# Kernel optimization log

Hardware: AMD Instinct MI355X
Metric: run time of the kernel (lower is better)

## Reference

```python
import jax, jax.numpy as jnp
import numpy as np

T, B, C = 512, 64, 512
ALPHA = 0.6        # blend coefficient from __init__
TAU = 10.0         # LIF tau
VTH = 1.0          # LIF v_threshold (v_reset = 0, hard reset)
BN_EPS = 1e-5


def spike_fn(x):
    # forward heaviside: spike = (v - v_th >= 0)
    return (x >= 0.0).astype(x.dtype)


def setup_inputs() -> dict:
    key = jax.random.key(0)
    ks = jax.random.split(key, 7)
    x = jax.random.normal(ks[0], (T, B, C), dtype=jnp.float32)
    conv_w = jax.random.normal(ks[1], (C, C, 3), dtype=jnp.float32) / np.sqrt(3.0 * C)
    conv_b = jax.random.normal(ks[2], (C,), dtype=jnp.float32) * 0.01
    bn_gamma = 0.5 + jax.random.uniform(ks[3], (C,), dtype=jnp.float32)
    bn_beta = jax.random.normal(ks[4], (C,), dtype=jnp.float32) * 0.1
    bn_mean = jax.random.normal(ks[5], (C,), dtype=jnp.float32) * 0.1
    bn_var = 0.5 + jax.random.uniform(ks[6], (C,), dtype=jnp.float32)
    return {"x": x, "conv_w": conv_w, "conv_b": conv_b,
            "bn_gamma": bn_gamma, "bn_beta": bn_beta,
            "bn_mean": bn_mean, "bn_var": bn_var}


def reference(x, conv_w, conv_b, bn_gamma, bn_beta, bn_mean, bn_var):
    # x: (T, B, C). Conv1d(k=3, pad=1) on a length-1 sequence reduces to a
    # dense matmul with the middle kernel tap: out = prev @ w[:,:,1].T + b.
    w1 = conv_w[:, :, 1]                      # (C_out, C_in)
    inv_std = bn_gamma * jax.lax.rsqrt(bn_var + BN_EPS)   # fused BN scale
    Bsz, Csz = x.shape[1], x.shape[2]

    def step(carry, x_t):
        prev, v = carry                        # prev: (B, C), v: (B, C) membrane
        conv = jnp.einsum('bc,dc->bd', prev, w1) + conv_b
        bn = (conv - bn_mean) * inv_std + bn_beta
        # LIF (decay_input=True, v_reset=0): v += (x - v) / tau
        v = v + (bn - v) / TAU
        s = spike_fn(v - VTH)
        v = v * (1.0 - s)                      # hard reset to 0
        new = (1.0 - ALPHA) * x_t + ALPHA * s  # alpha blend
        return (new, v), new                   # prev_state detached in torch; no-op for fwd

    init = (jnp.zeros((Bsz, Csz), x.dtype), jnp.zeros((Bsz, Csz), x.dtype))
    _, out = jax.lax.scan(step, init, x)       # out: (T, B, C)
    return out
```

## Files before the change

### kernel.cpp

```cpp
#include <hip/hip_runtime.h>
#include <stdint.h>

#define T_STEPS 512
#define BATCH 64
#define CH 512

using short8 = __attribute__((ext_vector_type(8))) short;
using f32x4  = __attribute__((ext_vector_type(4))) float;

__device__ __forceinline__ unsigned short f2b(float f) {
    union { float f; unsigned u; } c; c.f = f;
    unsigned r = (c.u + 0x7FFFu + ((c.u >> 16) & 1u)) >> 16;
    return (unsigned short)r;
}
__device__ __forceinline__ float b2f(unsigned short h) {
    union { unsigned u; float f; } c; c.u = ((unsigned)h) << 16;
    return c.f;
}

__global__ void prep(const float* __restrict__ cw, const float* __restrict__ cb,
                     const float* __restrict__ gamma, const float* __restrict__ beta,
                     const float* __restrict__ mean, const float* __restrict__ var,
                     unsigned short* __restrict__ wb,
                     float* __restrict__ wt,
                     float* __restrict__ isb,
                     float* __restrict__ k0p,
                     int* __restrict__ flag) {
    int idx = blockIdx.x * 256 + threadIdx.x;
    if (idx == 0) *flag = 0x7fffffff;
    if (idx >= CH * CH) return;
    int d = idx >> 9, c = idx & 511;
    float is = gamma[d] * rsqrtf(var[d] + 1e-5f);
    float w = cw[((size_t)d * CH + c) * 3 + 1];
    wb[idx] = f2b(0.04f * is * w);
    wt[(size_t)c * CH + d] = w;
    if (c == 0) {
        isb[d] = is;
        k0p[d] = 0.1f * ((cb[d] - mean[d]) * is + beta[d]);
    }
}

#define GBM 128
#define GBN 256
#define PADK 40

__global__ __launch_bounds__(512, 4) void gemm_fused(
    const float* __restrict__ Xp,
    const unsigned short* __restrict__ wbp,
    const float* __restrict__ k0p,
    unsigned short* __restrict__ Wbuf,
    float* __restrict__ outp,
    int Mc)
{
    __shared__ __align__(16) unsigned short As[2][GBM][PADK];
    __shared__ __align__(16) unsigned short Bs[2][GBN][PADK];
    int tid = threadIdx.x;
    int lane = tid & 63, wid = tid >> 6;
    int wm = wid >> 2, wn = wid & 3;
    int i0 = blockIdx.x * GBM;
    int n0 = blockIdx.y * GBN;
    int fm = lane & 15, fq = lane >> 4;
    int kq = fq * 8;
    bool wout = (blockIdx.y == 0);

    int ar = tid >> 2;
    int ak = (tid & 3) * 8;
    int brr = tid >> 1;
    int bk = (tid & 1) * 16;

    int grow = i0 + ar;
    bool arv = grow < Mc;
    int growc = arv ? grow : (Mc - 1);
    const float* xrow = &Xp[(size_t)growc * CH + ak];
    float* orow = &outp[(size_t)grow * CH + ak];
    const unsigned short* brow = &wbp[(size_t)(n0 + brr) * CH + bk];

    f32x4 acc[4][4] = {};

    {
        float4 a0 = *(const float4*)&xrow[0];
        float4 a1 = *(const float4*)&xrow[4];
        short8 av;
        av[0]=f2b(a0.x); av[1]=f2b(a0.y); av[2]=f2b(a0.z); av[3]=f2b(a0.w);
        av[4]=f2b(a1.x); av[5]=f2b(a1.y); av[6]=f2b(a1.z); av[7]=f2b(a1.w);
        *(short8*)&As[0][ar][ak] = av;
        short8 b0 = *(const short8*)&brow[0];
        short8 b1 = *(const short8*)&brow[8];
        *(short8*)&Bs[0][brr][bk]     = b0;
        *(short8*)&Bs[0][brr][bk + 8] = b1;
        if (wout && arv) {
            *(float4*)&orow[0] = make_float4(0.4f*a0.x, 0.4f*a0.y, 0.4f*a0.z, 0.4f*a0.w);
            *(float4*)&orow[4] = make_float4(0.4f*a1.x, 0.4f*a1.y, 0.4f*a1.z, 0.4f*a1.w);
        }
    }
    __syncthreads();

    for (int ks = 0; ks < 16; ++ks) {
        int cur = ks & 1;
        int kn = (ks + 1) * 32;
        float4 na0, na1;
        short8 nb0, nb1;
        if (kn < 512) {
            na0 = *(const float4*)&xrow[kn];
            na1 = *(const float4*)&xrow[kn + 4];
            nb0 = *(const short8*)&brow[kn];
            nb1 = *(const short8*)&brow[kn + 8];
        }
        short8 af[4], bfr[4];
        #pragma unroll
        for (int i = 0; i < 4; ++i)
            af[i] = *(const short8*)&As[cur][wm * 64 + i * 16 + fm][kq];
        #pragma unroll
        for (int j = 0; j < 4; ++j)
            bfr[j] = *(const short8*)&Bs[cur][wn * 64 + j * 16 + fm][kq];
        #pragma unroll
        for (int i = 0; i < 4; ++i)
            #pragma unroll
            for (int j = 0; j < 4; ++j)
                acc[i][j] = __builtin_amdgcn_mfma_f32_16x16x32_bf16(af[i], bfr[j], acc[i][j], 0, 0, 0);
        if (kn < 512) {
            short8 av;
            av[0]=f2b(na0.x); av[1]=f2b(na0.y); av[2]=f2b(na0.z); av[3]=f2b(na0.w);
            av[4]=f2b(na1.x); av[5]=f2b(na1.y); av[6]=f2b(na1.z); av[7]=f2b(na1.w);
            *(short8*)&As[cur ^ 1][ar][ak] = av;
            *(short8*)&Bs[cur ^ 1][brr][bk]     = nb0;
            *(short8*)&Bs[cur ^ 1][brr][bk + 8] = nb1;
            if (wout && arv) {
                *(float4*)&orow[kn]     = make_float4(0.4f*na0.x, 0.4f*na0.y, 0.4f*na0.z, 0.4f*na0.w);
                *(float4*)&orow[kn + 4] = make_float4(0.4f*na1.x, 0.4f*na1.y, 0.4f*na1.z, 0.4f*na1.w);
            }
        }
        __syncthreads();
    }

    float b0e[4];
    #pragma unroll
    for (int j = 0; j < 4; ++j) b0e[j] = k0p[n0 + wn * 64 + j * 16 + fm];
    #pragma unroll
    for (int i = 0; i < 4; ++i)
        #pragma unroll
        for (int r = 0; r < 4; ++r) {
            int row = i0 + wm * 64 + i * 16 + fq * 4 + r;
            if (row < Mc) {
                #pragma unroll
                for (int j = 0; j < 4; ++j) {
                    int col = n0 + wn * 64 + j * 16 + fm;
                    Wbuf[(size_t)row * CH + col] = f2b(acc[i][j][r] + b0e[j]);
                }
            }
        }
}

__device__ __forceinline__ short8 wload(const unsigned short* Wbuf, int t, int a0, int b, int c0) {
    int r = t - 1 - a0; if (r < 0) r = 0;
    return *(const short8*)&Wbuf[((size_t)r * BATCH + b) * CH + c0];
}

__global__ __launch_bounds__(512) void scan_all(
    const unsigned short* __restrict__ Wbuf,
    const float* __restrict__ k0p,
    const float* __restrict__ vcin,
    float* __restrict__ vcout,
    int* __restrict__ flag,
    int t0, int a0, int segs, int chunk_idx)
{
    const float F = 1.1790184577738595e-3f;
    __shared__ float Ssh[8][CH];
    int b = blockIdx.x;
    int wid = threadIdx.x >> 6;
    int lane = threadIdx.x & 63;
    int c0 = lane * 8;
    int seg = wid;
    bool active = seg < segs;
    int tstart = t0 + seg * 64;

    float B0[8];
    #pragma unroll
    for (int k = 0; k < 8; ++k) B0[k] = k0p[c0 + k];

    if (active) {
        float S[8] = {};
        short8 pz[4];
        #pragma unroll
        for (int p = 0; p < 4; ++p) pz[p] = wload(Wbuf, tstart + p, a0, b, c0);
        for (int ii = 0; ii < 64; ii += 4) {
            #pragma unroll
            for (int p = 0; p < 4; ++p) {
                int t = tstart + ii + p;
                short8 zv = pz[p];
                int tn = ii + p + 4;
                if (tn < 64) pz[p] = wload(Wbuf, tstart + tn, a0, b, c0);
                #pragma unroll
                for (int k = 0; k < 8; ++k) {
                    float wv = (t == 0) ? B0[k] : b2f((unsigned short)zv[k]);
                    S[k] = fmaf(0.9f, S[k], wv);
                }
            }
        }
        #pragma unroll
        for (int k = 0; k < 8; ++k) Ssh[seg][c0 + k] = S[k];
    }
    __syncthreads();

    float v[8];
    if (t0 == 0) {
        #pragma unroll
        for (int k = 0; k < 8; ++k) v[k] = 0.0f;
    } else {
        const float* vp = &vcin[(size_t)b * CH + c0];
        float4 v0 = *(const float4*)&vp[0], v1 = *(const float4*)&vp[4];
        v[0]=v0.x; v[1]=v0.y; v[2]=v0.z; v[3]=v0.w; v[4]=v1.x; v[5]=v1.y; v[6]=v1.z; v[7]=v1.w;
    }
    for (int u = 0; u < seg; ++u) {
        #pragma unroll
        for (int k = 0; k < 8; ++k) v[k] = fmaf(v[k], F, Ssh[u][c0 + k]);
    }

    if (active) {
        bool anyhit = false;
        short8 pz[4];
        #pragma unroll
        for (int p = 0; p < 4; ++p) pz[p] = wload(Wbuf, tstart + p, a0, b, c0);
        for (int ii = 0; ii < 64; ii += 4) {
            #pragma unroll
            for (int p = 0; p < 4; ++p) {
                int t = tstart + ii + p;
                short8 zv = pz[p];
                int tn = ii + p + 4;
                if (tn < 64) pz[p] = wload(Wbuf, tstart + tn, a0, b, c0);
                float m = -1e30f;
                #pragma unroll
                for (int k = 0; k < 8; ++k) {
                    float wv = (t == 0) ? B0[k] : b2f((unsigned short)zv[k]);
                    v[k] = fmaf(0.9f, v[k], wv);
                    m = fmaxf(m, v[k]);
                }
                anyhit |= (m >= 0.995f);
            }
        }
        if (__ballot(anyhit) != 0ULL && lane == 0) atomicMin(flag, chunk_idx);
        if (seg == segs - 1) {
            float* vp = &vcout[(size_t)b * CH + c0];
            *(float4*)&vp[0] = make_float4(v[0], v[1], v[2], v[3]);
            *(float4*)&vp[4] = make_float4(v[4], v[5], v[6], v[7]);
        }
    }
}

__global__ __launch_bounds__(64) void seq_fix(
    const float* __restrict__ x,
    const float* __restrict__ wt,
    const unsigned short* __restrict__ Wbuf,
    const float* __restrict__ isb,
    const float* __restrict__ k0p,
    const int* __restrict__ flag,
    const float* __restrict__ vcin,
    float* __restrict__ out,
    float* __restrict__ v_state,
    unsigned long long* __restrict__ s_state,
    int t0, int t1, int a0, int chunk_idx, int save_state)
{
    int fl = *flag;
    if (fl > chunk_idx) return;
    int b = blockIdx.x;
    int lane = threadIdx.x;
    int c0 = lane * 8;

    float is6[8], B0[8];
    #pragma unroll
    for (int k = 0; k < 8; ++k) {
        is6[k] = 0.06f * isb[c0 + k];
        B0[k]  = k0p[c0 + k];
    }

    float v[8];
    unsigned long long mk[8];
    if (t0 == 0) {
        #pragma unroll
        for (int k = 0; k < 8; ++k) v[k] = 0.0f;
        #pragma unroll
        for (int j = 0; j < 8; ++j) mk[j] = 0ULL;
    } else if (fl == chunk_idx) {
        #pragma unroll
        for (int k = 0; k < 8; ++k) v[k] = vcin[(size_t)b * CH + c0 + k];
        #pragma unroll
        for (int j = 0; j < 8; ++j) mk[j] = 0ULL;
    } else {
        #pragma unroll
        for (int k = 0; k < 8; ++k) v[k] = v_state[(size_t)b * CH + c0 + k];
        #pragma unroll
        for (int j = 0; j < 8; ++j) mk[j] = s_state[b * 8 + j];
    }

    float xc[8]; short8 wc;
    {
        const float4* xp = (const float4*)&x[((size_t)t0 * BATCH + b) * CH + c0];
        float4 x0 = xp[0], x1 = xp[1];
        xc[0]=x0.x; xc[1]=x0.y; xc[2]=x0.z; xc[3]=x0.w; xc[4]=x1.x; xc[5]=x1.y; xc[6]=x1.z; xc[7]=x1.w;
        wc = wload(Wbuf, t0, a0, b, c0);
    }
    for (int t = t0; t < t1; ++t) {
        float xn[8]; short8 wn_;
        if (t + 1 < t1) {
            const float4* xp = (const float4*)&x[((size_t)(t + 1) * BATCH + b) * CH + c0];
            float4 x0 = xp[0], x1 = xp[1];
            xn[0]=x0.x; xn[1]=x0.y; xn[2]=x0.z; xn[3]=x0.w; xn[4]=x1.x; xn[5]=x1.y; xn[6]=x1.z; xn[7]=x1.w;
            wn_ = wload(Wbuf, t + 1, a0, b, c0);
        }
        float acc[8] = {};
        unsigned long long anym = mk[0]|mk[1]|mk[2]|mk[3]|mk[4]|mk[5]|mk[6]|mk[7];
        if (anym) {
            #pragma unroll
            for (int j = 0; j < 8; ++j) {
                unsigned long long m = mk[j];
                while (m) {
                    int l = __builtin_ctzll(m); m &= m - 1;
                    const float4* wr = (const float4*)&wt[(size_t)(l * 8 + j) * CH + c0];
                    float4 w0 = wr[0], w1 = wr[1];
                    acc[0]+=w0.x; acc[1]+=w0.y; acc[2]+=w0.z; acc[3]+=w0.w;
                    acc[4]+=w1.x; acc[5]+=w1.y; acc[6]+=w1.z; acc[7]+=w1.w;
                }
            }
        }
        bool s[8];
        #pragma unroll
        for (int k = 0; k < 8; ++k) {
            float wv = (t == 0) ? B0[k] : b2f((unsigned short)wc[k]);
            float vv = fmaf(0.9f, v[k], fmaf(is6[k], acc[k], wv));
            s[k] = (vv >= 1.0f);
            v[k] = s[k] ? 0.0f : vv;
        }
        float4* op = (float4*)&out[((size_t)t * BATCH + b) * CH + c0];
        op[0] = make_float4(fmaf(0.4f,xc[0],s[0]?0.6f:0.f), fmaf(0.4f,xc[1],s[1]?0.6f:0.f),
                            fmaf(0.4f,xc[2],s[2]?0.6f:0.f), fmaf(0.4f,xc[3],s[3]?0.6f:0.f));
        op[1] = make_float4(fmaf(0.4f,xc[4],s[4]?0.6f:0.f), fmaf(0.4f,xc[5],s[5]?0.6f:0.f),
                            fmaf(0.4f,xc[6],s[6]?0.6f:0.f), fmaf(0.4f,xc[7],s[7]?0.6f:0.f));
        #pragma unroll
        for (int j = 0; j < 8; ++j) mk[j] = __ballot(s[j]);
        #pragma unroll
        for (int k = 0; k < 8; ++k) xc[k] = xn[k];
        wc = wn_;
    }
    if (save_state) {
        #pragma unroll
        for (int k = 0; k < 8; ++k) v_state[(size_t)b * CH + c0 + k] = v[k];
        if (lane < 8) s_state[b * 8 + lane] = mk[lane];
    }
}

extern "C" void kernel_launch(void* const* d_in, const int* in_sizes, int n_in,
                              void* d_out, int out_size, void* d_ws, size_t ws_size,
                              hipStream_t stream) {
    const float* x     = (const float*)d_in[0];
    const float* cw    = (const float*)d_in[1];
    const float* cb    = (const float*)d_in[2];
    const float* gamma = (const float*)d_in[3];
    const float* beta  = (const float*)d_in[4];
    const float* mean  = (const float*)d_in[5];
    const float* var   = (const float*)d_in[6];
    float* out = (float*)d_out;

    char* ws = (char*)d_ws;
    size_t off = 0;
    auto alloc = [&](size_t bytes) -> char* {
        char* p = ws + off;
        off = (off + bytes + 255) & ~(size_t)255;
        return p;
    };
    unsigned short* wb = (unsigned short*)alloc((size_t)CH * CH * 2);
    float* wt  = (float*)alloc((size_t)CH * CH * 4);
    float* isb = (float*)alloc(CH * 4);
    float* k0p = (float*)alloc(CH * 4);
    int* flag  = (int*)alloc(256);
    float* vst = (float*)alloc((size_t)BATCH * CH * 4);
    unsigned long long* sst = (unsigned long long*)alloc(BATCH * 8 * 8);
    float* vca = (float*)alloc((size_t)BATCH * CH * 4);
    float* vcb = (float*)alloc((size_t)BATCH * CH * 4);
    unsigned short* Wbuf = (unsigned short*)(ws + off);

    size_t avail = (ws_size > off) ? ws_size - off : 0;
    long rows = (long)(avail / ((size_t)BATCH * CH * 2));
    long cs = ((rows - 1) / 64) * 64;
    if (cs > T_STEPS) cs = T_STEPS;
    if (cs < 64) cs = 64;
    int CS = (int)cs;

    hipLaunchKernelGGL(prep, dim3((CH * CH + 255) / 256), dim3(256), 0, stream,
                       cw, cb, gamma, beta, mean, var, wb, wt, isb, k0p, flag);

    float *vin = vca, *vout = vcb;
    int k = 0;
    for (int t0 = 0; t0 < T_STEPS; t0 += CS, ++k) {
        int t1 = t0 + CS; if (t1 > T_STEPS) t1 = T_STEPS;
        int a0 = (t0 == 0) ? 0 : t0 - 1;
        int gend = (t1 == T_STEPS) ? T_STEPS : t1 - 1;
        int Mc = (gend - a0) * BATCH;
        hipLaunchKernelGGL(gemm_fused, dim3((Mc + GBM - 1) / GBM, 2), dim3(512), 0, stream,
                           x + (size_t)a0 * BATCH * CH, wb, k0p, Wbuf,
                           out + (size_t)a0 * BATCH * CH, Mc);
        int segs = (t1 - t0) / 64;
        hipLaunchKernelGGL(scan_all, dim3(BATCH), dim3(512), 0, stream,
                           Wbuf, k0p, vin, vout, flag, t0, a0, segs, k);
        hipLaunchKernelGGL(seq_fix, dim3(BATCH), dim3(64), 0, stream,
                           x, wt, Wbuf, isb, k0p, flag, vin, out, vst, sst,
                           t0, t1, a0, k, (t1 < T_STEPS) ? 1 : 0);
        float* tmp = vin; vin = vout; vout = tmp;
    }
}
```

Measured before the change: 77.47 us.

## Widen GEMM tile to full N and replace scan second pass with prefix-max bound

The GEMM now covers all 512 output columns per block, so each X row is loaded and converted to bf16 once instead of twice, at the cost of a doubled accumulator set and larger LDS with lower occupancy. The scan kernel drops its second sequential pass over Wbuf. It tracks a running max of the zero-start partial sum, bounds the threshold check with 0.9*max(v,0)+P, and computes the end state as v*F+S. The bound is conservative and could flag extra chunks for the sequential fix path. The bf16 conversion also switches to the HIP intrinsic.

Result: slower. 276.7 us (+257.2%).

```diff
diff --git a/kernel.cpp b/kernel.cpp
--- a/kernel.cpp
+++ b/kernel.cpp
@@ -1,4 +1,5 @@
 #include <hip/hip_runtime.h>
+#include <hip/hip_bf16.h>
 #include <stdint.h>
 
 #define T_STEPS 512
@@ -9,9 +10,9 @@
 using f32x4  = __attribute__((ext_vector_type(4))) float;
 
 __device__ __forceinline__ unsigned short f2b(float f) {
-    union { float f; unsigned u; } c; c.f = f;
-    unsigned r = (c.u + 0x7FFFu + ((c.u >> 16) & 1u)) >> 16;
-    return (unsigned short)r;
+    union { __hip_bfloat16 h; unsigned short u; } c;
+    c.h = __float2bfloat16(f);
+    return c.u;
 }
 __device__ __forceinline__ float b2f(unsigned short h) {
     union { unsigned u; float f; } c; c.u = ((unsigned)h) << 16;
@@ -41,10 +42,9 @@
 }
 
 #define GBM 128
-#define GBN 256
 #define PADK 40
 
-__global__ __launch_bounds__(512, 4) void gemm_fused(
+__global__ __launch_bounds__(512, 2) void gemm_fused(
     const float* __restrict__ Xp,
     const unsigned short* __restrict__ wbp,
     const float* __restrict__ k0p,
@@ -53,44 +53,45 @@
     int Mc)
 {
     __shared__ __align__(16) unsigned short As[2][GBM][PADK];
-    __shared__ __align__(16) unsigned short Bs[2][GBN][PADK];
+    __shared__ __align__(16) unsigned short Bs[2][512][PADK];
     int tid = threadIdx.x;
     int lane = tid & 63, wid = tid >> 6;
     int wm = wid >> 2, wn = wid & 3;
     int i0 = blockIdx.x * GBM;
-    int n0 = blockIdx.y * GBN;
     int fm = lane & 15, fq = lane >> 4;
     int kq = fq * 8;
-    bool wout = (blockIdx.y == 0);
 
     int ar = tid >> 2;
     int ak = (tid & 3) * 8;
-    int brr = tid >> 1;
-    int bk = (tid & 1) * 16;
 
     int grow = i0 + ar;
     bool arv = grow < Mc;
     int growc = arv ? grow : (Mc - 1);
     const float* xrow = &Xp[(size_t)growc * CH + ak];
     float* orow = &outp[(size_t)grow * CH + ak];
-    const unsigned short* brow = &wbp[(size_t)(n0 + brr) * CH + bk];
-
-    f32x4 acc[4][4] = {};
+    const unsigned short* brow = &wbp[(size_t)ar * CH + ak];
+
+    f32x4 acc[4][8] = {};
+
+    float4 sa0, sa1;
+    short8 sb[4];
 
     {
-        float4 a0 = *(const float4*)&xrow[0];
-        float4 a1 = *(const float4*)&xrow[4];
+        sa0 = *(const float4*)&xrow[0];
+        sa1 = *(const float4*)&xrow[4];
+        #pragma unroll
+        for (int p = 0; p < 4; ++p)
+            sb[p] = *(const short8*)&brow[(size_t)p * 128 * CH];
         short8 av;
-        av[0]=f2b(a0.x); av[1]=f2b(a0.y); av[2]=f2b(a0.z); av[3]=f2b(a0.w);
-        av[4]=f2b(a1.x); av[5]=f2b(a1.y); av[6]=f2b(a1.z); av[7]=f2b(a1.w);
+        av[0]=f2b(sa0.x); av[1]=f2b(sa0.y); av[2]=f2b(sa0.z); av[3]=f2b(sa0.w);
+        av[4]=f2b(sa1.x); av[5]=f2b(sa1.y); av[6]=f2b(sa1.z); av[7]=f2b(sa1.w);
         *(short8*)&As[0][ar][ak] = av;
-        short8 b0 = *(const short8*)&brow[0];
-        short8 b1 = *(const short8*)&brow[8];
-        *(short8*)&Bs[0][brr][bk]     = b0;
-        *(short8*)&Bs[0][brr][bk + 8] = b1;
-        if (wout && arv) {
-            *(float4*)&orow[0] = make_float4(0.4f*a0.x, 0.4f*a0.y, 0.4f*a0.z, 0.4f*a0.w);
-            *(float4*)&orow[4] = make_float4(0.4f*a1.x, 0.4f*a1.y, 0.4f*a1.z, 0.4f*a1.w);
+        #pragma unroll
+        for (int p = 0; p < 4; ++p)
+            *(short8*)&Bs[0][ar + p * 128][ak] = sb[p];
+        if (arv) {
+            *(float4*)&orow[0] = make_float4(0.4f*sa0.x, 0.4f*sa0.y, 0.4f*sa0.z, 0.4f*sa0.w);
+            *(float4*)&orow[4] = make_float4(0.4f*sa1.x, 0.4f*sa1.y, 0.4f*sa1.z, 0.4f*sa1.w);
         }
     }
     __syncthreads();
@@ -98,44 +99,44 @@
     for (int ks = 0; ks < 16; ++ks) {
         int cur = ks & 1;
         int kn = (ks + 1) * 32;
-        float4 na0, na1;
-        short8 nb0, nb1;
         if (kn < 512) {
-            na0 = *(const float4*)&xrow[kn];
-            na1 = *(const float4*)&xrow[kn + 4];
-            nb0 = *(const short8*)&brow[kn];
-            nb1 = *(const short8*)&brow[kn + 8];
-        }
-        short8 af[4], bfr[4];
+            sa0 = *(const float4*)&xrow[kn];
+            sa1 = *(const float4*)&xrow[kn + 4];
+            #pragma unroll
+            for (int p = 0; p < 4; ++p)
+                sb[p] = *(const short8*)&brow[(size_t)p * 128 * CH + kn];
+        }
+        short8 af[4], bfr[8];
         #pragma unroll
         for (int i = 0; i < 4; ++i)
             af[i] = *(const short8*)&As[cur][wm * 64 + i * 16 + fm][kq];
         #pragma unroll
-        for (int j = 0; j < 4; ++j)
-            bfr[j] = *(const short8*)&Bs[cur][wn * 64 + j * 16 + fm][kq];
+        for (int j = 0; j < 8; ++j)
+            bfr[j] = *(const short8*)&Bs[cur][wn * 128 + j * 16 + fm][kq];
         #pragma unroll
         for (int i = 0; i < 4; ++i)
             #pragma unroll
-            for (int j = 0; j < 4; ++j)
+            for (int j = 0; j < 8; ++j)
                 acc[i][j] = __builtin_amdgcn_mfma_f32_16x16x32_bf16(af[i], bfr[j], acc[i][j], 0, 0, 0);
         if (kn < 512) {
             short8 av;
-            av[0]=f2b(na0.x); av[1]=f2b(na0.y); av[2]=f2b(na0.z); av[3]=f2b(na0.w);
-            av[4]=f2b(na1.x); av[5]=f2b(na1.y); av[6]=f2b(na1.z); av[7]=f2b(na1.w);
+            av[0]=f2b(sa0.x); av[1]=f2b(sa0.y); av[2]=f2b(sa0.z); av[3]=f2b(sa0.w);
+            av[4]=f2b(sa1.x); av[5]=f2b(sa1.y); av[6]=f2b(sa1.z); av[7]=f2b(sa1.w);
             *(short8*)&As[cur ^ 1][ar][ak] = av;
-            *(short8*)&Bs[cur ^ 1][brr][bk]     = nb0;
-            *(short8*)&Bs[cur ^ 1][brr][bk + 8] = nb1;
-            if (wout && arv) {
-                *(float4*)&orow[kn]     = make_float4(0.4f*na0.x, 0.4f*na0.y, 0.4f*na0.z, 0.4f*na0.w);
-                *(float4*)&orow[kn + 4] = make_float4(0.4f*na1.x, 0.4f*na1.y, 0.4f*na1.z, 0.4f*na1.w);
+            #pragma unroll
+            for (int p = 0; p < 4; ++p)
+                *(short8*)&Bs[cur ^ 1][ar + p * 128][ak] = sb[p];
+            if (arv) {
+                *(float4*)&orow[kn]     = make_float4(0.4f*sa0.x, 0.4f*sa0.y, 0.4f*sa0.z, 0.4f*sa0.w);
+                *(float4*)&orow[kn + 4] = make_float4(0.4f*sa1.x, 0.4f*sa1.y, 0.4f*sa1.z, 0.4f*sa1.w);
             }
         }
         __syncthreads();
     }
 
-    float b0e[4];
-    #pragma unroll
-    for (int j = 0; j < 4; ++j) b0e[j] = k0p[n0 + wn * 64 + j * 16 + fm];
+    float b0e[8];
+    #pragma unroll
+    for (int j = 0; j < 8; ++j) b0e[j] = k0p[wn * 128 + j * 16 + fm];
     #pragma unroll
     for (int i = 0; i < 4; ++i)
         #pragma unroll
@@ -143,8 +144,8 @@
             int row = i0 + wm * 64 + i * 16 + fq * 4 + r;
             if (row < Mc) {
                 #pragma unroll
-                for (int j = 0; j < 4; ++j) {
-                    int col = n0 + wn * 64 + j * 16 + fm;
+                for (int j = 0; j < 8; ++j) {
+                    int col = wn * 128 + j * 16 + fm;
                     Wbuf[(size_t)row * CH + col] = f2b(acc[i][j][r] + b0e[j]);
                 }
             }
@@ -167,10 +168,9 @@
     const float F = 1.1790184577738595e-3f;
     __shared__ float Ssh[8][CH];
     int b = blockIdx.x;
-    int wid = threadIdx.x >> 6;
+    int seg = threadIdx.x >> 6;
     int lane = threadIdx.x & 63;
     int c0 = lane * 8;
-    int seg = wid;
     bool active = seg < segs;
     int tstart = t0 + seg * 64;
 
@@ -178,8 +178,11 @@
     #pragma unroll
     for (int k = 0; k < 8; ++k) B0[k] = k0p[c0 + k];
 
+    float S[8] = {};
+    float P[8];
+    #pragma unroll
+    for (int k = 0; k < 8; ++k) P[k] = -1e30f;
     if (active) {
-        float S[8] = {};
         short8 pz[4];
         #pragma unroll
         for (int p = 0; p < 4; ++p) pz[p] = wload(Wbuf, tstart + p, a0, b, c0);
@@ -194,6 +197,7 @@
                 for (int k = 0; k < 8; ++k) {
                     float wv = (t == 0) ? B0[k] : b2f((unsigned short)zv[k]);
                     S[k] = fmaf(0.9f, S[k], wv);
+                    P[k] = fmaxf(P[k], S[k]);
                 }
             }
         }
@@ -217,32 +221,18 @@
     }
 
     if (active) {
-        bool anyhit = false;
-        short8 pz[4];
-        #pragma unroll
-        for (int p = 0; p < 4; ++p) pz[p] = wload(Wbuf, tstart + p, a0, b, c0);
-        for (int ii = 0; ii < 64; ii += 4) {
-            #pragma unroll
-            for (int p = 0; p < 4; ++p) {
-                int t = tstart + ii + p;
-                short8 zv = pz[p];
-                int tn = ii + p + 4;
-                if (tn < 64) pz[p] = wload(Wbuf, tstart + tn, a0, b, c0);
-                float m = -1e30f;
-                #pragma unroll
-                for (int k = 0; k < 8; ++k) {
-                    float wv = (t == 0) ? B0[k] : b2f((unsigned short)zv[k]);
-                    v[k] = fmaf(0.9f, v[k], wv);
-                    m = fmaxf(m, v[k]);
-                }
-                anyhit |= (m >= 0.995f);
-            }
-        }
-        if (__ballot(anyhit) != 0ULL && lane == 0) atomicMin(flag, chunk_idx);
+        bool hit = false;
+        #pragma unroll
+        for (int k = 0; k < 8; ++k)
+            hit |= (fmaf(0.9f, fmaxf(v[k], 0.0f), P[k]) >= 0.995f);
+        if (__ballot(hit) != 0ULL && lane == 0) atomicMin(flag, chunk_idx);
         if (seg == segs - 1) {
             float* vp = &vcout[(size_t)b * CH + c0];
-            *(float4*)&vp[0] = make_float4(v[0], v[1], v[2], v[3]);
-            *(float4*)&vp[4] = make_float4(v[4], v[5], v[6], v[7]);
+            float ve[8];
+            #pragma unroll
+            for (int k = 0; k < 8; ++k) ve[k] = fmaf(v[k], F, S[k]);
+            *(float4*)&vp[0] = make_float4(ve[0], ve[1], ve[2], ve[3]);
+            *(float4*)&vp[4] = make_float4(ve[4], ve[5], ve[6], ve[7]);
         }
     }
 }
@@ -395,7 +385,7 @@
         int a0 = (t0 == 0) ? 0 : t0 - 1;
         int gend = (t1 == T_STEPS) ? T_STEPS : t1 - 1;
         int Mc = (gend - a0) * BATCH;
-        hipLaunchKernelGGL(gemm_fused, dim3((Mc + GBM - 1) / GBM, 2), dim3(512), 0, stream,
+        hipLaunchKernelGGL(gemm_fused, dim3((Mc + GBM - 1) / GBM), dim3(512), 0, stream,
                            x + (size_t)a0 * BATCH * CH, wb, k0p, Wbuf,
                            out + (size_t)a0 * BATCH * CH, Mc);
         int segs = (t1 - t0) / 64;
```
